# Optimization experiments

Measured on AMD Instinct MI355X. Metric: run time of the kernel, lower is better.

The kernel has to match this reference:

```python
import jax, jax.numpy as jnp
import numpy as np

N_NODES = 100000
N_EDGES = 1600000


def _norms(src, dst, n_nodes, dtype):
    # DGL GraphConv norm='both': scale src by out-degree^{-1/2}, dst by in-degree^{-1/2}
    ones = jnp.ones((src.shape[0],), dtype=dtype)
    deg_out = jax.ops.segment_sum(ones, src, num_segments=n_nodes)
    deg_in = jax.ops.segment_sum(ones, dst, num_segments=n_nodes)
    inv_sqrt_out = jnp.where(deg_out > 0, jax.lax.rsqrt(jnp.maximum(deg_out, 1.0)), 0.0)
    inv_sqrt_in = jnp.where(deg_in > 0, jax.lax.rsqrt(jnp.maximum(deg_in, 1.0)), 0.0)
    return inv_sqrt_out, inv_sqrt_in


def _graph_conv(x, W, src, dst, inv_sqrt_out, inv_sqrt_in, n_nodes, relu):
    # norm='both': out = D_in^{-1/2} A D_out^{-1/2} x W
    h = x * inv_sqrt_out[:, None]
    h = h @ W                      # dense transform before aggregation
    msg = h[src]                   # gather messages along edges [E, F]
    agg = jax.ops.segment_sum(msg, dst, num_segments=n_nodes)
    out = agg * inv_sqrt_in[:, None]
    return jax.nn.relu(out) if relu else out


def setup_inputs() -> dict:
    key = jax.random.key(0)
    k1, k2, k3, k4, k5, k6 = jax.random.split(key, 6)
    in_dim, h_dim, out_dim = 128, 128, 64
    features = jax.random.normal(k1, (N_NODES, in_dim), dtype=jnp.float32)
    W1 = jax.random.normal(k2, (in_dim, h_dim), dtype=jnp.float32) * (1.0 / np.sqrt(in_dim))
    W2 = jax.random.normal(k3, (h_dim, h_dim), dtype=jnp.float32) * (1.0 / np.sqrt(h_dim))
    W3 = jax.random.normal(k4, (h_dim, out_dim), dtype=jnp.float32) * (1.0 / np.sqrt(h_dim))
    src = jax.random.randint(k5, (N_EDGES,), 0, N_NODES, dtype=jnp.int32)
    dst = jax.random.randint(k6, (N_EDGES,), 0, N_NODES, dtype=jnp.int32)
    return {"features": features, "W1": W1, "W2": W2, "W3": W3, "src": src, "dst": dst}


def reference(features, W1, W2, W3, src, dst):
    inv_sqrt_out, inv_sqrt_in = _norms(src, dst, N_NODES, features.dtype)
    h = _graph_conv(features, W1, src, dst, inv_sqrt_out, inv_sqrt_in, N_NODES, relu=True)
    h = _graph_conv(h, W2, src, dst, inv_sqrt_out, inv_sqrt_in, N_NODES, relu=True)
    h = _graph_conv(h, W3, src, dst, inv_sqrt_out, inv_sqrt_in, N_NODES, relu=False)
    return h
```

## Files before the change

### kernel.cpp

```cpp
#include <hip/hip_runtime.h>


typedef float f32x4 __attribute__((ext_vector_type(4)));
typedef __bf16 bf16x8 __attribute__((ext_vector_type(8)));

constexpr int CAP = 5120;
constexpr int MAXNB = 400;

__device__ inline unsigned short f2bf_bits(float f) {
    unsigned u = __float_as_uint(f);
    unsigned r = u + 0x7fff + ((u >> 16) & 1);
    return (unsigned short)(r >> 16);
}
__device__ inline float bf_bits2f(unsigned short s) {
    return __uint_as_float(((unsigned)s) << 16);
}
__device__ inline float bf_lo(unsigned v) { return __uint_as_float(v << 16); }
__device__ inline float bf_hi(unsigned v) { return __uint_as_float(v & 0xffff0000u); }


__global__ __launch_bounds__(512) void bucket_scatter(
    const int* __restrict__ src, const int* __restrict__ dst,
    int* __restrict__ cur_d, int* __restrict__ cur_s,
    int* __restrict__ bpair, int* __restrict__ bsrc, int E, int NB) {
    __shared__ int hd[MAXNB], hs[MAXNB], bd[MAXNB], bs[MAXNB];
    const int tid = threadIdx.x;
    for (int i = tid; i < NB; i += 512) { hd[i] = 0; hs[i] = 0; }
    __syncthreads();

    const int base = (blockIdx.x * 512 + tid) * 8;
    int s[8], d[8], rd[8], rs[8];
    bool va[8];
    if (base + 8 <= E) {
        const int4 s0 = *(const int4*)(src + base);
        const int4 s1 = *(const int4*)(src + base + 4);
        const int4 d0 = *(const int4*)(dst + base);
        const int4 d1 = *(const int4*)(dst + base + 4);
        s[0] = s0.x; s[1] = s0.y; s[2] = s0.z; s[3] = s0.w;
        s[4] = s1.x; s[5] = s1.y; s[6] = s1.z; s[7] = s1.w;
        d[0] = d0.x; d[1] = d0.y; d[2] = d0.z; d[3] = d0.w;
        d[4] = d1.x; d[5] = d1.y; d[6] = d1.z; d[7] = d1.w;
#pragma unroll
        for (int j = 0; j < 8; ++j) va[j] = true;
    } else {
#pragma unroll
        for (int j = 0; j < 8; ++j) {
            const int e = base + j;
            va[j] = e < E;
            const int ec = va[j] ? e : 0;
            s[j] = src[ec];
            d[j] = dst[ec];
        }
    }
#pragma unroll
    for (int j = 0; j < 8; ++j) {
        if (va[j]) {
            rd[j] = atomicAdd(&hd[d[j] >> 8], 1);
            rs[j] = atomicAdd(&hs[s[j] >> 8], 1);
        }
    }
    __syncthreads();
    for (int i = tid; i < NB; i += 512) {
        bd[i] = hd[i] ? atomicAdd(&cur_d[i], hd[i]) : 0;
        bs[i] = hs[i] ? atomicAdd(&cur_s[i], hs[i]) : 0;
    }
    __syncthreads();
#pragma unroll
    for (int j = 0; j < 8; ++j) {
        if (va[j]) {
            const int b = d[j] >> 8;
            const int pos = bd[b] + rd[j];
            if (pos < CAP) bpair[(size_t)b * CAP + pos] = (s[j] << 8) | (d[j] & 255);
            const int c = s[j] >> 8;
            const int ps = bs[c] + rs[j];
            if (ps < CAP) bsrc[(size_t)c * CAP + ps] = s[j];
        }
    }
}

__global__ __launch_bounds__(256) void csr_outdeg(
    const int* __restrict__ bpair, const int* __restrict__ bsrc,
    const int* __restrict__ bcnt_d, const int* __restrict__ bcnt_s,
    int* __restrict__ row_ptr, int* __restrict__ col,
    float* __restrict__ isi, float* __restrict__ iso,
    float* __restrict__ fscale, int N, int NB) {
    __shared__ int h[256], hs[256], sc[256], cur[256], red[256];
    const int b = blockIdx.x;
    const int tid = threadIdx.x;
    const int cnt = min(bcnt_d[b], CAP);
    const int scnt = min(bcnt_s[b], CAP);

    int partial = 0;
    for (int i = tid; i < b; i += 256) partial += bcnt_d[i];
    red[tid] = partial;
    __syncthreads();
#pragma unroll
    for (int off = 128; off > 0; off >>= 1) {
        if (tid < off) red[tid] += red[tid + off];
        __syncthreads();
    }
    const int base = red[0];

    const int* pairs = bpair + (size_t)b * CAP;
    const int* svals = bsrc + (size_t)b * CAP;
    h[tid] = 0;
    hs[tid] = 0;
    __syncthreads();
    for (int i = tid; i < cnt; i += 256) atomicAdd(&h[pairs[i] & 255], 1);
    for (int i = tid; i < scnt; i += 256) atomicAdd(&hs[svals[i] & 255], 1);
    __syncthreads();
    sc[tid] = h[tid];
    __syncthreads();
    for (int off = 1; off < 256; off <<= 1) {
        int v = (tid >= off) ? sc[tid - off] : 0;
        __syncthreads();
        sc[tid] += v;
        __syncthreads();
    }
    const int lp = sc[tid] - h[tid];
    const int node = b * 256 + tid;
    if (node < N) {
        row_ptr[node] = base + lp;
        const float di = (h[tid] > 0) ? rsqrtf((float)h[tid]) : 0.f;
        const float dw = (hs[tid] > 0) ? rsqrtf((float)hs[tid]) : 0.f;
        isi[node] = di;
        iso[node] = dw;
        fscale[node] = di * dw;
    }
    if (b == NB - 1 && tid == 0) row_ptr[N] = base + cnt;
    cur[tid] = lp;
    __syncthreads();
    for (int i = tid; i < cnt; i += 256) {
        const int p = pairs[i];
        const int pos = base + atomicAdd(&cur[p & 255], 1);
        col[pos] = p >> 8;
    }
}


__device__ inline void wpack1(const float* W, unsigned short* Wh,
                              unsigned short* Wl, int t, int F) {
    const int n = t >> 7, k = t & 127;
    const float w = W[k * F + n];
    const unsigned short hb = f2bf_bits(w);
    Wh[t] = hb;
    Wl[t] = f2bf_bits(w - bf_bits2f(hb));
}

__global__ __launch_bounds__(256) void wpack_all(
    const float* __restrict__ W1, const float* __restrict__ W2,
    const float* __restrict__ W3, unsigned short* __restrict__ Wt1h,
    unsigned short* __restrict__ Wt1l, unsigned short* __restrict__ Wt2h,
    unsigned short* __restrict__ Wt2l, unsigned short* __restrict__ Wt3h,
    unsigned short* __restrict__ Wt3l, int* __restrict__ cur_zero) {
    int t = blockIdx.x * 256 + threadIdx.x;
    if (t < 2 * MAXNB) cur_zero[t] = 0;
    if (t < 16384) {
        wpack1(W1, Wt1h, Wt1l, t, 128);
    } else if (t < 32768) {
        wpack1(W2, Wt2h, Wt2l, t - 16384, 128);
    } else if (t < 40960) {
        wpack1(W3, Wt3h, Wt3l, t - 32768, 64);
    }
}


template <int F>
__global__ __launch_bounds__(256) void gemm_mfma(
    const float* __restrict__ X, const unsigned short* __restrict__ Wt_hi,
    const unsigned short* __restrict__ Wt_lo, const float* __restrict__ so,
    unsigned short* __restrict__ Y, int N) {
    constexpr int NT = F / 16;
    const int wave = threadIdx.x >> 6;
    const int lane = threadIdx.x & 63;
    const int r0 = blockIdx.x * 128 + wave * 32;
    const int l15 = lane & 15;
    const int quad = lane >> 4;

    const int rowA0 = min(r0 + l15, N - 1);
    const int rowA1 = min(r0 + 16 + l15, N - 1);
    const float s0 = so[rowA0];
    const float s1 = so[rowA1];
    const float* pX0 = X + (size_t)rowA0 * 128 + quad * 8;
    const float* pX1 = X + (size_t)rowA1 * 128 + quad * 8;

    f32x4 acc0[NT], acc1[NT];
    const f32x4 z = {0.f, 0.f, 0.f, 0.f};
#pragma unroll
    for (int t = 0; t < NT; ++t) { acc0[t] = z; acc1[t] = z; }

    union AB { bf16x8 v; unsigned short u[8]; unsigned u32[4]; };

#pragma unroll
    for (int s = 0; s < 4; ++s) {
        const int kb = s * 32;
        AB bh[NT], bl[NT];
#pragma unroll
        for (int t = 0; t < NT; ++t) {
            const int n = t * 16 + l15;
            bh[t].v = *(const bf16x8*)(Wt_hi + n * 128 + kb + quad * 8);
            bl[t].v = *(const bf16x8*)(Wt_lo + n * 128 + kb + quad * 8);
        }
        float a[8];
        *(f32x4*)&a[0] = *(const f32x4*)(pX0 + kb);
        *(f32x4*)&a[4] = *(const f32x4*)(pX0 + kb + 4);
        AB ah, al;
#pragma unroll
        for (int j = 0; j < 8; j += 2) {
            const float x0 = a[j] * s0;
            const float x1 = a[j + 1] * s0;
            const float h0 = __uint_as_float(__float_as_uint(x0) & 0xffff0000u);
            const float h1 = __uint_as_float(__float_as_uint(x1) & 0xffff0000u);
            const float l0 = x0 - h0;
            const float l1 = x1 - h1;
            ah.u32[j >> 1] = __builtin_amdgcn_perm(
                __float_as_uint(x1), __float_as_uint(x0), 0x07060302u);
            al.u32[j >> 1] = __builtin_amdgcn_perm(
                __float_as_uint(l1), __float_as_uint(l0), 0x07060302u);
        }
#pragma unroll
        for (int t = 0; t < NT; ++t) {
            acc0[t] = __builtin_amdgcn_mfma_f32_16x16x32_bf16(ah.v, bh[t].v, acc0[t], 0, 0, 0);
            acc0[t] = __builtin_amdgcn_mfma_f32_16x16x32_bf16(al.v, bh[t].v, acc0[t], 0, 0, 0);
            acc0[t] = __builtin_amdgcn_mfma_f32_16x16x32_bf16(ah.v, bl[t].v, acc0[t], 0, 0, 0);
        }
        *(f32x4*)&a[0] = *(const f32x4*)(pX1 + kb);
        *(f32x4*)&a[4] = *(const f32x4*)(pX1 + kb + 4);
#pragma unroll
        for (int j = 0; j < 8; j += 2) {
            const float x0 = a[j] * s1;
            const float x1 = a[j + 1] * s1;
            const float h0 = __uint_as_float(__float_as_uint(x0) & 0xffff0000u);
            const float h1 = __uint_as_float(__float_as_uint(x1) & 0xffff0000u);
            const float l0 = x0 - h0;
            const float l1 = x1 - h1;
            ah.u32[j >> 1] = __builtin_amdgcn_perm(
                __float_as_uint(x1), __float_as_uint(x0), 0x07060302u);
            al.u32[j >> 1] = __builtin_amdgcn_perm(
                __float_as_uint(l1), __float_as_uint(l0), 0x07060302u);
        }
#pragma unroll
        for (int t = 0; t < NT; ++t) {
            acc1[t] = __builtin_amdgcn_mfma_f32_16x16x32_bf16(ah.v, bh[t].v, acc1[t], 0, 0, 0);
            acc1[t] = __builtin_amdgcn_mfma_f32_16x16x32_bf16(al.v, bh[t].v, acc1[t], 0, 0, 0);
            acc1[t] = __builtin_amdgcn_mfma_f32_16x16x32_bf16(ah.v, bl[t].v, acc1[t], 0, 0, 0);
        }
    }

#pragma unroll
    for (int t = 0; t < NT; ++t) {
#pragma unroll
        for (int r = 0; r < 4; ++r) {
            int node0 = r0 + quad * 4 + r;
            if (node0 < N) Y[(size_t)node0 * F + t * 16 + l15] = f2bf_bits(acc0[t][r]);
            int node1 = r0 + 16 + quad * 4 + r;
            if (node1 < N) Y[(size_t)node1 * F + t * 16 + l15] = f2bf_bits(acc1[t][r]);
        }
    }
}


template <int F>
__global__ __launch_bounds__(256) void fused_gather_gemm(
    const unsigned short* __restrict__ msg, const int* __restrict__ row_ptr,
    const int* __restrict__ col, const float* __restrict__ fscale,
    const unsigned short* __restrict__ Wt_hi, const unsigned short* __restrict__ Wt_lo,
    unsigned short* __restrict__ Yout, int N) {
    __shared__ __align__(16) unsigned Asw[32 * 64];
    const int wave = threadIdx.x >> 6;
    const int lane = threadIdx.x & 63;
    const int d0 = blockIdx.x * 32;
    const unsigned* m32 = (const unsigned*)msg;

#pragma unroll 1
    for (int i = 0; i < 8; ++i) {
        const int r = wave * 8 + i;
        const int d = d0 + r;
        float a0 = 0.f, a1 = 0.f, b0 = 0.f, b1 = 0.f;
        if (d < N) {
            const int start = row_ptr[d], end = row_ptr[d + 1];
            int e = start;
            const int efull = start + ((end - start) & ~7);
            for (; e < efull; e += 8) {
                int c[8];
#pragma unroll
                for (int j = 0; j < 8; ++j) c[j] = col[e + j];
                unsigned v[8];
#pragma unroll
                for (int j = 0; j < 8; ++j)
                    v[j] = m32[(unsigned)c[j] * 64u + (unsigned)lane];
#pragma unroll
                for (int j = 0; j < 8; j += 2) {
                    a0 += bf_lo(v[j]);     a1 += bf_hi(v[j]);
                    b0 += bf_lo(v[j + 1]); b1 += bf_hi(v[j + 1]);
                }
            }
            const int rem = end - e;
            if (rem > 0) {
                int c[8];
#pragma unroll
                for (int j = 0; j < 8; ++j) c[j] = col[e + min(j, rem - 1)];
                unsigned v[8];
#pragma unroll
                for (int j = 0; j < 8; ++j)
                    v[j] = m32[(unsigned)c[j] * 64u + (unsigned)lane];
#pragma unroll
                for (int j = 0; j < 8; ++j) {
                    a0 += (j < rem) ? bf_lo(v[j]) : 0.f;
                    a1 += (j < rem) ? bf_hi(v[j]) : 0.f;
                }
            }
            const float sc = fscale[d];
            a0 = fmaxf((a0 + b0) * sc, 0.f);
            a1 = fmaxf((a1 + b1) * sc, 0.f);
        }
        const unsigned packed =
            ((unsigned)f2bf_bits(a1) << 16) | (unsigned)f2bf_bits(a0);
        Asw[r * 64 + (lane ^ ((r & 7) << 2))] = packed;
    }
    __syncthreads();

    constexpr int CT = F / 64;
    const int l15 = lane & 15;
    const int quad = lane >> 4;
    const int cbase = wave * (F / 4);

    f32x4 acc[2][CT];
    const f32x4 z = {0.f, 0.f, 0.f, 0.f};
#pragma unroll
    for (int rt = 0; rt < 2; ++rt)
#pragma unroll
        for (int bt = 0; bt < CT; ++bt) acc[rt][bt] = z;

#pragma unroll
    for (int s = 0; s < 4; ++s) {
        bf16x8 a[2];
#pragma unroll
        for (int rt = 0; rt < 2; ++rt) {
            const int row = rt * 16 + l15;
            const int dw = (s * 16 + quad * 4) ^ ((row & 7) << 2);
            a[rt] = *(const bf16x8*)&Asw[row * 64 + dw];
        }
        bf16x8 bh[CT], bl[CT];
#pragma unroll
        for (int bt = 0; bt < CT; ++bt) {
            const int n = cbase + bt * 16 + l15;
            bh[bt] = *(const bf16x8*)(Wt_hi + n * 128 + s * 32 + quad * 8);
            bl[bt] = *(const bf16x8*)(Wt_lo + n * 128 + s * 32 + quad * 8);
        }
#pragma unroll
        for (int rt = 0; rt < 2; ++rt)
#pragma unroll
            for (int bt = 0; bt < CT; ++bt) {
                acc[rt][bt] = __builtin_amdgcn_mfma_f32_16x16x32_bf16(a[rt], bh[bt], acc[rt][bt], 0, 0, 0);
                acc[rt][bt] = __builtin_amdgcn_mfma_f32_16x16x32_bf16(a[rt], bl[bt], acc[rt][bt], 0, 0, 0);
            }
    }

#pragma unroll
    for (int rt = 0; rt < 2; ++rt)
#pragma unroll
        for (int bt = 0; bt < CT; ++bt) {
#pragma unroll
            for (int r = 0; r < 4; ++r) {
                const int node = d0 + rt * 16 + quad * 4 + r;
                if (node < N)
                    Yout[(size_t)node * F + cbase + bt * 16 + l15] =
                        f2bf_bits(acc[rt][bt][r]);
            }
        }
}


__global__ __launch_bounds__(256) void gather64(
    const unsigned short* __restrict__ msg, const int* __restrict__ row_ptr,
    const int* __restrict__ col, const float* __restrict__ isi,
    float* __restrict__ out, int N) {
    const int w = (blockIdx.x * 256 + threadIdx.x) >> 6;
    const int lane = threadIdx.x & 63;
    const int node = w * 2 + (lane >> 5);
    const int j31 = lane & 31;
    if (node >= N) return;
    const int start = row_ptr[node], end = row_ptr[node + 1];
    const unsigned* m32 = (const unsigned*)msg;

    float a0 = 0.f, a1 = 0.f, b0 = 0.f, b1 = 0.f;
    int e = start;
    const int efull = start + ((end - start) & ~7);
    for (; e < efull; e += 8) {
        int c[8];
#pragma unroll
        for (int j = 0; j < 8; ++j) c[j] = col[e + j];
        unsigned v[8];
#pragma unroll
        for (int j = 0; j < 8; ++j)
            v[j] = m32[(unsigned)c[j] * 32u + (unsigned)j31];
#pragma unroll
        for (int j = 0; j < 8; j += 2) {
            a0 += bf_lo(v[j]);     a1 += bf_hi(v[j]);
            b0 += bf_lo(v[j + 1]); b1 += bf_hi(v[j + 1]);
        }
    }
    const int rem = end - e;
    if (rem > 0) {
        int c[8];
#pragma unroll
        for (int j = 0; j < 8; ++j) c[j] = col[e + min(j, rem - 1)];
        unsigned v[8];
#pragma unroll
        for (int j = 0; j < 8; ++j)
            v[j] = m32[(unsigned)c[j] * 32u + (unsigned)j31];
#pragma unroll
        for (int j = 0; j < 8; ++j) {
            a0 += (j < rem) ? bf_lo(v[j]) : 0.f;
            a1 += (j < rem) ? bf_hi(v[j]) : 0.f;
        }
    }
    const float sc = isi[node];
    *(float2*)(out + (size_t)node * 64 + j31 * 2) =
        make_float2((a0 + b0) * sc, (a1 + b1) * sc);
}


extern "C" void kernel_launch(void* const* d_in, const int* in_sizes, int n_in,
                              void* d_out, int out_size, void* d_ws, size_t ws_size,
                              hipStream_t stream) {
    const float* features = (const float*)d_in[0];
    const float* W1 = (const float*)d_in[1];
    const float* W2 = (const float*)d_in[2];
    const float* W3 = (const float*)d_in[3];
    const int* src = (const int*)d_in[4];
    const int* dst = (const int*)d_in[5];
    float* out = (float*)d_out;

    const int N = in_sizes[0] / 128;
    const int E = in_sizes[4];
    const int NB = (N + 255) >> 8;

    char* ws = (char*)d_ws;
    unsigned short* A = (unsigned short*)ws;      ws += (size_t)N * 128 * 2;
    unsigned short* Y = (unsigned short*)ws;      ws += (size_t)N * 128 * 2;
    int* row_ptr = (int*)ws;                      ws += (size_t)(N + 1) * 4;
    int* col = (int*)ws;                          ws += (size_t)E * 4;
    float* iso = (float*)ws;                      ws += (size_t)N * 4;
    float* isi = (float*)ws;                      ws += (size_t)N * 4;
    float* fscale = (float*)ws;                   ws += (size_t)N * 4;
    int* cur_d = (int*)ws;                        ws += MAXNB * 4;
    int* cur_s = (int*)ws;                        ws += MAXNB * 4;
    unsigned short* Wt1h = (unsigned short*)ws;   ws += 128 * 128 * 2;
    unsigned short* Wt1l = (unsigned short*)ws;   ws += 128 * 128 * 2;
    unsigned short* Wt2h = (unsigned short*)ws;   ws += 128 * 128 * 2;
    unsigned short* Wt2l = (unsigned short*)ws;   ws += 128 * 128 * 2;
    unsigned short* Wt3h = (unsigned short*)ws;   ws += 64 * 128 * 2;
    unsigned short* Wt3l = (unsigned short*)ws;   ws += 64 * 128 * 2;

    int* bpair = (int*)A;
    int* bsrc = (int*)((char*)A + (size_t)MAXNB * CAP * 4);

    wpack_all<<<160, 256, 0, stream>>>(W1, W2, W3, Wt1h, Wt1l, Wt2h, Wt2l,
                                       Wt3h, Wt3l, cur_d);
    const int gBS = (E + 4095) / 4096;
    bucket_scatter<<<gBS, 512, 0, stream>>>(src, dst, cur_d, cur_s, bpair, bsrc, E, NB);
    csr_outdeg<<<NB, 256, 0, stream>>>(bpair, bsrc, cur_d, cur_s, row_ptr,
                                       col, isi, iso, fscale, N, NB);

    const int gG = (N + 127) / 128;
    const int gF = (N + 31) / 32;
    const int ga64 = ((N / 2 + 1) * 64 + 255) / 256;

    gemm_mfma<128><<<gG, 256, 0, stream>>>(features, Wt1h, Wt1l, iso, Y, N);
    fused_gather_gemm<128><<<gF, 256, 0, stream>>>(Y, row_ptr, col, fscale,
                                                   Wt2h, Wt2l, A, N);
    fused_gather_gemm<64><<<gF, 256, 0, stream>>>(A, row_ptr, col, fscale,
                                                  Wt3h, Wt3l, Y, N);
    gather64<<<ga64, 256, 0, stream>>>(Y, row_ptr, col, isi, out, N);
}
```

Before: 373.7 us.

## Split out-degree kernel and co-schedule CSR build with first-layer GEMM

The combined CSR/degree kernel is split in two. A small src_iso kernel computes out-degree norms first. The CSR construction (row_ptr, col, isi, fscale) then runs in the same launch as the first-layer MFMA GEMM, using disjoint block ranges, so the two independent stages can overlap on the GPU and one launch is saved. The cost is an extra small kernel that reads bsrc on its own pass, plus a heavier fused kernel whose register needs are set by the GEMM path.

```diff
diff --git a/kernel.cpp b/kernel.cpp
--- a/kernel.cpp
+++ b/kernel.cpp
@@ -78,62 +78,170 @@
     }
 }
 
-__global__ __launch_bounds__(256) void csr_outdeg(
-    const int* __restrict__ bpair, const int* __restrict__ bsrc,
-    const int* __restrict__ bcnt_d, const int* __restrict__ bcnt_s,
-    int* __restrict__ row_ptr, int* __restrict__ col,
-    float* __restrict__ isi, float* __restrict__ iso,
-    float* __restrict__ fscale, int N, int NB) {
-    __shared__ int h[256], hs[256], sc[256], cur[256], red[256];
+__global__ __launch_bounds__(256) void src_iso(
+    const int* __restrict__ bsrc, const int* __restrict__ bcnt_s,
+    float* __restrict__ iso, int N, int NB) {
+    __shared__ int hs[256];
     const int b = blockIdx.x;
     const int tid = threadIdx.x;
-    const int cnt = min(bcnt_d[b], CAP);
     const int scnt = min(bcnt_s[b], CAP);
-
-    int partial = 0;
-    for (int i = tid; i < b; i += 256) partial += bcnt_d[i];
-    red[tid] = partial;
-    __syncthreads();
-#pragma unroll
-    for (int off = 128; off > 0; off >>= 1) {
-        if (tid < off) red[tid] += red[tid + off];
+    const int* svals = bsrc + (size_t)b * CAP;
+    hs[tid] = 0;
+    __syncthreads();
+    for (int i = tid; i < scnt; i += 256) atomicAdd(&hs[svals[i] & 255], 1);
+    __syncthreads();
+    const int node = b * 256 + tid;
+    if (node < N)
+        iso[node] = (hs[tid] > 0) ? rsqrtf((float)hs[tid]) : 0.f;
+}
+
+
+__global__ __launch_bounds__(256) void csr_plus_gemm(
+    const int* __restrict__ bpair, const int* __restrict__ bcnt_d,
+    int* __restrict__ row_ptr, int* __restrict__ col,
+    const float* __restrict__ iso, float* __restrict__ isi,
+    float* __restrict__ fscale,
+    const float* __restrict__ X, const unsigned short* __restrict__ Wt_hi,
+    const unsigned short* __restrict__ Wt_lo, unsigned short* __restrict__ Y,
+    int N, int NB) {
+    __shared__ int h[256], sc[256], cur[256], red[256];
+    const int tid = threadIdx.x;
+
+    if (blockIdx.x < (unsigned)NB) {
+        const int b = blockIdx.x;
+        const int cnt = min(bcnt_d[b], CAP);
+
+        int partial = 0;
+        for (int i = tid; i < b; i += 256) partial += bcnt_d[i];
+        red[tid] = partial;
         __syncthreads();
-    }
-    const int base = red[0];
-
-    const int* pairs = bpair + (size_t)b * CAP;
-    const int* svals = bsrc + (size_t)b * CAP;
-    h[tid] = 0;
-    hs[tid] = 0;
-    __syncthreads();
-    for (int i = tid; i < cnt; i += 256) atomicAdd(&h[pairs[i] & 255], 1);
-    for (int i = tid; i < scnt; i += 256) atomicAdd(&hs[svals[i] & 255], 1);
-    __syncthreads();
-    sc[tid] = h[tid];
-    __syncthreads();
-    for (int off = 1; off < 256; off <<= 1) {
-        int v = (tid >= off) ? sc[tid - off] : 0;
+#pragma unroll
+        for (int off = 128; off > 0; off >>= 1) {
+            if (tid < off) red[tid] += red[tid + off];
+            __syncthreads();
+        }
+        const int base = red[0];
+
+        const int* pairs = bpair + (size_t)b * CAP;
+        h[tid] = 0;
         __syncthreads();
-        sc[tid] += v;
+        for (int i = tid; i < cnt; i += 256) atomicAdd(&h[pairs[i] & 255], 1);
         __syncthreads();
-    }
-    const int lp = sc[tid] - h[tid];
-    const int node = b * 256 + tid;
-    if (node < N) {
-        row_ptr[node] = base + lp;
-        const float di = (h[tid] > 0) ? rsqrtf((float)h[tid]) : 0.f;
-        const float dw = (hs[tid] > 0) ? rsqrtf((float)hs[tid]) : 0.f;
-        isi[node] = di;
-        iso[node] = dw;
-        fscale[node] = di * dw;
-    }
-    if (b == NB - 1 && tid == 0) row_ptr[N] = base + cnt;
-    cur[tid] = lp;
-    __syncthreads();
-    for (int i = tid; i < cnt; i += 256) {
-        const int p = pairs[i];
-        const int pos = base + atomicAdd(&cur[p & 255], 1);
-        col[pos] = p >> 8;
+        sc[tid] = h[tid];
+        __syncthreads();
+        for (int off = 1; off < 256; off <<= 1) {
+            int v = (tid >= off) ? sc[tid - off] : 0;
+            __syncthreads();
+            sc[tid] += v;
+            __syncthreads();
+        }
+        const int lp = sc[tid] - h[tid];
+        const int node = b * 256 + tid;
+        if (node < N) {
+            row_ptr[node] = base + lp;
+            const float di = (h[tid] > 0) ? rsqrtf((float)h[tid]) : 0.f;
+            isi[node] = di;
+            fscale[node] = di * iso[node];
+        }
+        if (b == NB - 1 && tid == 0) row_ptr[N] = base + cnt;
+        cur[tid] = lp;
+        __syncthreads();
+        for (int i = tid; i < cnt; i += 256) {
+            const int p = pairs[i];
+            const int pos = base + atomicAdd(&cur[p & 255], 1);
+            col[pos] = p >> 8;
+        }
+        return;
+    }
+
+    constexpr int F = 128;
+    constexpr int NT = F / 16;
+    const int bid = blockIdx.x - NB;
+    const int wave = tid >> 6;
+    const int lane = tid & 63;
+    const int r0 = bid * 128 + wave * 32;
+    const int l15 = lane & 15;
+    const int quad = lane >> 4;
+
+    const int rowA0 = min(r0 + l15, N - 1);
+    const int rowA1 = min(r0 + 16 + l15, N - 1);
+    const float s0 = iso[rowA0];
+    const float s1 = iso[rowA1];
+    const float* pX0 = X + (size_t)rowA0 * 128 + quad * 8;
+    const float* pX1 = X + (size_t)rowA1 * 128 + quad * 8;
+
+    f32x4 acc0[NT], acc1[NT];
+    const f32x4 z = {0.f, 0.f, 0.f, 0.f};
+#pragma unroll
+    for (int t = 0; t < NT; ++t) { acc0[t] = z; acc1[t] = z; }
+
+    union AB { bf16x8 v; unsigned short u[8]; unsigned u32[4]; };
+
+#pragma unroll
+    for (int s = 0; s < 4; ++s) {
+        const int kb = s * 32;
+        AB bh[NT], bl[NT];
+#pragma unroll
+        for (int t = 0; t < NT; ++t) {
+            const int n = t * 16 + l15;
+            bh[t].v = *(const bf16x8*)(Wt_hi + n * 128 + kb + quad * 8);
+            bl[t].v = *(const bf16x8*)(Wt_lo + n * 128 + kb + quad * 8);
+        }
+        float a[8];
+        *(f32x4*)&a[0] = *(const f32x4*)(pX0 + kb);
+        *(f32x4*)&a[4] = *(const f32x4*)(pX0 + kb + 4);
+        AB ah, al;
+#pragma unroll
+        for (int j = 0; j < 8; j += 2) {
+            const float x0 = a[j] * s0;
+            const float x1 = a[j + 1] * s0;
+            const float h0 = __uint_as_float(__float_as_uint(x0) & 0xffff0000u);
+            const float h1 = __uint_as_float(__float_as_uint(x1) & 0xffff0000u);
+            const float l0 = x0 - h0;
+            const float l1 = x1 - h1;
+            ah.u32[j >> 1] = __builtin_amdgcn_perm(
+                __float_as_uint(x1), __float_as_uint(x0), 0x07060302u);
+            al.u32[j >> 1] = __builtin_amdgcn_perm(
+                __float_as_uint(l1), __float_as_uint(l0), 0x07060302u);
+        }
+#pragma unroll
+        for (int t = 0; t < NT; ++t) {
+            acc0[t] = __builtin_amdgcn_mfma_f32_16x16x32_bf16(ah.v, bh[t].v, acc0[t], 0, 0, 0);
+            acc0[t] = __builtin_amdgcn_mfma_f32_16x16x32_bf16(al.v, bh[t].v, acc0[t], 0, 0, 0);
+            acc0[t] = __builtin_amdgcn_mfma_f32_16x16x32_bf16(ah.v, bl[t].v, acc0[t], 0, 0, 0);
+        }
+        *(f32x4*)&a[0] = *(const f32x4*)(pX1 + kb);
+        *(f32x4*)&a[4] = *(const f32x4*)(pX1 + kb + 4);
+#pragma unroll
+        for (int j = 0; j < 8; j += 2) {
+            const float x0 = a[j] * s1;
+            const float x1 = a[j + 1] * s1;
+            const float h0 = __uint_as_float(__float_as_uint(x0) & 0xffff0000u);
+            const float h1 = __uint_as_float(__float_as_uint(x1) & 0xffff0000u);
+            const float l0 = x0 - h0;
+            const float l1 = x1 - h1;
+            ah.u32[j >> 1] = __builtin_amdgcn_perm(
+                __float_as_uint(x1), __float_as_uint(x0), 0x07060302u);
+            al.u32[j >> 1] = __builtin_amdgcn_perm(
+                __float_as_uint(l1), __float_as_uint(l0), 0x07060302u);
+        }
+#pragma unroll
+        for (int t = 0; t < NT; ++t) {
+            acc1[t] = __builtin_amdgcn_mfma_f32_16x16x32_bf16(ah.v, bh[t].v, acc1[t], 0, 0, 0);
+            acc1[t] = __builtin_amdgcn_mfma_f32_16x16x32_bf16(al.v, bh[t].v, acc1[t], 0, 0, 0);
+            acc1[t] = __builtin_amdgcn_mfma_f32_16x16x32_bf16(ah.v, bl[t].v, acc1[t], 0, 0, 0);
+        }
+    }
+
+#pragma unroll
+    for (int t = 0; t < NT; ++t) {
+#pragma unroll
+        for (int r = 0; r < 4; ++r) {
+            int node0 = r0 + quad * 4 + r;
+            if (node0 < N) Y[(size_t)node0 * F + t * 16 + l15] = f2bf_bits(acc0[t][r]);
+            int node1 = r0 + 16 + quad * 4 + r;
+            if (node1 < N) Y[(size_t)node1 * F + t * 16 + l15] = f2bf_bits(acc1[t][r]);
+        }
     }
 }
 
@@ -161,101 +269,6 @@
         wpack1(W2, Wt2h, Wt2l, t - 16384, 128);
     } else if (t < 40960) {
         wpack1(W3, Wt3h, Wt3l, t - 32768, 64);
-    }
-}
-
-
-template <int F>
-__global__ __launch_bounds__(256) void gemm_mfma(
-    const float* __restrict__ X, const unsigned short* __restrict__ Wt_hi,
-    const unsigned short* __restrict__ Wt_lo, const float* __restrict__ so,
-    unsigned short* __restrict__ Y, int N) {
-    constexpr int NT = F / 16;
-    const int wave = threadIdx.x >> 6;
-    const int lane = threadIdx.x & 63;
-    const int r0 = blockIdx.x * 128 + wave * 32;
-    const int l15 = lane & 15;
-    const int quad = lane >> 4;
-
-    const int rowA0 = min(r0 + l15, N - 1);
-    const int rowA1 = min(r0 + 16 + l15, N - 1);
-    const float s0 = so[rowA0];
-    const float s1 = so[rowA1];
-    const float* pX0 = X + (size_t)rowA0 * 128 + quad * 8;
-    const float* pX1 = X + (size_t)rowA1 * 128 + quad * 8;
-
-    f32x4 acc0[NT], acc1[NT];
-    const f32x4 z = {0.f, 0.f, 0.f, 0.f};
-#pragma unroll
-    for (int t = 0; t < NT; ++t) { acc0[t] = z; acc1[t] = z; }
-
-    union AB { bf16x8 v; unsigned short u[8]; unsigned u32[4]; };
-
-#pragma unroll
-    for (int s = 0; s < 4; ++s) {
-        const int kb = s * 32;
-        AB bh[NT], bl[NT];
-#pragma unroll
-        for (int t = 0; t < NT; ++t) {
-            const int n = t * 16 + l15;
-            bh[t].v = *(const bf16x8*)(Wt_hi + n * 128 + kb + quad * 8);
-            bl[t].v = *(const bf16x8*)(Wt_lo + n * 128 + kb + quad * 8);
-        }
-        float a[8];
-        *(f32x4*)&a[0] = *(const f32x4*)(pX0 + kb);
-        *(f32x4*)&a[4] = *(const f32x4*)(pX0 + kb + 4);
-        AB ah, al;
-#pragma unroll
-        for (int j = 0; j < 8; j += 2) {
-            const float x0 = a[j] * s0;
-            const float x1 = a[j + 1] * s0;
-            const float h0 = __uint_as_float(__float_as_uint(x0) & 0xffff0000u);
-            const float h1 = __uint_as_float(__float_as_uint(x1) & 0xffff0000u);
-            const float l0 = x0 - h0;
-            const float l1 = x1 - h1;
-            ah.u32[j >> 1] = __builtin_amdgcn_perm(
-                __float_as_uint(x1), __float_as_uint(x0), 0x07060302u);
-            al.u32[j >> 1] = __builtin_amdgcn_perm(
-                __float_as_uint(l1), __float_as_uint(l0), 0x07060302u);
-        }
-#pragma unroll
-        for (int t = 0; t < NT; ++t) {
-            acc0[t] = __builtin_amdgcn_mfma_f32_16x16x32_bf16(ah.v, bh[t].v, acc0[t], 0, 0, 0);
-            acc0[t] = __builtin_amdgcn_mfma_f32_16x16x32_bf16(al.v, bh[t].v, acc0[t], 0, 0, 0);
-            acc0[t] = __builtin_amdgcn_mfma_f32_16x16x32_bf16(ah.v, bl[t].v, acc0[t], 0, 0, 0);
-        }
-        *(f32x4*)&a[0] = *(const f32x4*)(pX1 + kb);
-        *(f32x4*)&a[4] = *(const f32x4*)(pX1 + kb + 4);
-#pragma unroll
-        for (int j = 0; j < 8; j += 2) {
-            const float x0 = a[j] * s1;
-            const float x1 = a[j + 1] * s1;
-            const float h0 = __uint_as_float(__float_as_uint(x0) & 0xffff0000u);
-            const float h1 = __uint_as_float(__float_as_uint(x1) & 0xffff0000u);
-            const float l0 = x0 - h0;
-            const float l1 = x1 - h1;
-            ah.u32[j >> 1] = __builtin_amdgcn_perm(
-                __float_as_uint(x1), __float_as_uint(x0), 0x07060302u);
-            al.u32[j >> 1] = __builtin_amdgcn_perm(
-                __float_as_uint(l1), __float_as_uint(l0), 0x07060302u);
-        }
-#pragma unroll
-        for (int t = 0; t < NT; ++t) {
-            acc1[t] = __builtin_amdgcn_mfma_f32_16x16x32_bf16(ah.v, bh[t].v, acc1[t], 0, 0, 0);
-            acc1[t] = __builtin_amdgcn_mfma_f32_16x16x32_bf16(al.v, bh[t].v, acc1[t], 0, 0, 0);
-            acc1[t] = __builtin_amdgcn_mfma_f32_16x16x32_bf16(ah.v, bl[t].v, acc1[t], 0, 0, 0);
-        }
-    }
-
-#pragma unroll
-    for (int t = 0; t < NT; ++t) {
-#pragma unroll
-        for (int r = 0; r < 4; ++r) {
-            int node0 = r0 + quad * 4 + r;
-            if (node0 < N) Y[(size_t)node0 * F + t * 16 + l15] = f2bf_bits(acc0[t][r]);
-            int node1 = r0 + 16 + quad * 4 + r;
-            if (node1 < N) Y[(size_t)node1 * F + t * 16 + l15] = f2bf_bits(acc1[t][r]);
-        }
     }
 }
 
@@ -461,14 +474,16 @@
                                        Wt3h, Wt3l, cur_d);
     const int gBS = (E + 4095) / 4096;
     bucket_scatter<<<gBS, 512, 0, stream>>>(src, dst, cur_d, cur_s, bpair, bsrc, E, NB);
-    csr_outdeg<<<NB, 256, 0, stream>>>(bpair, bsrc, cur_d, cur_s, row_ptr,
-                                       col, isi, iso, fscale, N, NB);
+    src_iso<<<NB, 256, 0, stream>>>(bsrc, cur_s, iso, N, NB);
 
     const int gG = (N + 127) / 128;
+    csr_plus_gemm<<<NB + gG, 256, 0, stream>>>(bpair, cur_d, row_ptr, col,
+                                               iso, isi, fscale, features,
+                                               Wt1h, Wt1l, Y, N, NB);
+
     const int gF = (N + 31) / 32;
     const int ga64 = ((N / 2 + 1) * 64 + 255) / 256;
 
-    gemm_mfma<128><<<gG, 256, 0, stream>>>(features, Wt1h, Wt1l, iso, Y, N);
     fused_gather_gemm<128><<<gF, 256, 0, stream>>>(Y, row_ptr, col, fscale,
                                                    Wt2h, Wt2l, A, N);
     fused_gather_gemm<64><<<gF, 256, 0, stream>>>(A, row_ptr, col, fscale,
```

After: 371.1 us. Within noise of the previous version (-0.7%).
